# Kernel optimization log

Hardware: AMD Instinct MI355X
Metric: run time of the kernel (lower is better)

Reference implementation:

```python
import jax, jax.numpy as jnp
import numpy as np

N, IN_DIM, OUT_DIM, HEADS = 3072, 512, 64, 8
EDGE_PROB = 0.01
NEG_SLOPE = 0.2


def setup_inputs() -> dict:
    key = jax.random.key(0)
    k1, k2, k3, k4, k5 = jax.random.split(key, 5)
    x = jax.random.normal(k1, (N, IN_DIM), dtype=jnp.float32)
    # sparse-ish dense adjacency mask with self-loops
    adj = (jax.random.uniform(k2, (N, N)) < EDGE_PROB).astype(jnp.float32)
    adj = jnp.maximum(adj, jnp.eye(N, dtype=jnp.float32))
    W = jax.random.normal(k3, (HEADS, IN_DIM, OUT_DIM), dtype=jnp.float32) * 0.1
    a_src = jax.random.normal(k4, (HEADS, OUT_DIM), dtype=jnp.float32) * 0.1
    a_dst = jax.random.normal(k5, (HEADS, OUT_DIM), dtype=jnp.float32) * 0.1
    return {"x": x, "adj": adj, "W": W, "a_src": a_src, "a_dst": a_dst}


def reference(x, adj, W, a_src, a_dst):
    # per-head linear projection: [H, N, OUT]
    h = jnp.einsum("ni,hio->hno", x, W)
    # attention logits e_ij = LeakyReLU(a_src . h_i + a_dst . h_j)
    f_src = jnp.einsum("hno,ho->hn", h, a_src)  # [H, N]
    f_dst = jnp.einsum("hno,ho->hn", h, a_dst)  # [H, N]
    e = f_src[:, :, None] + f_dst[:, None, :]   # [H, N, N]
    e = jax.nn.leaky_relu(e, negative_slope=NEG_SLOPE)
    # mask non-edges, row-softmax over neighbors
    e = jnp.where(adj[None] > 0, e, jnp.float32(-1e9))
    att = jax.nn.softmax(e, axis=-1)             # [H, N, N]
    # aggregate neighbor features per head
    out = jnp.einsum("hij,hjo->hio", att, h)     # [H, N, OUT]
    # concat heads along feature dim -> [N, H*OUT]
    return out.transpose(1, 0, 2).reshape(N, HEADS * OUT_DIM)
```

## Files before the change

### kernel.cpp

```cpp
#include <hip/hip_runtime.h>

#define N_NODES 3072
#define IN_DIM 512
#define OUT_DIM 64
#define HEADS 8
#define NEG_SLOPE 0.2f
#define MAX_E 128

typedef __attribute__((ext_vector_type(8))) short bf16x8;
typedef __attribute__((ext_vector_type(4))) float f32x4;

#define XFRAG_TILES (N_NODES / 16)
#define KTILES (IN_DIM / 32)
#define XFRAG_THREADS (XFRAG_TILES * KTILES * 64)
#define WFRAG_THREADS (HEADS * KTILES * 4 * 64)

__device__ inline unsigned short f2bf(float f) {
    union { float f; unsigned u; } v; v.f = f;
    unsigned r = (v.u + 0x7FFF + ((v.u >> 16) & 1)) >> 16;
    return (unsigned short)r;
}

__global__ __launch_bounds__(256) void gat_prep(
    const float* __restrict__ x, const float* __restrict__ W,
    short* __restrict__ xfrag, short* __restrict__ wfrag) {
    int tid = blockIdx.x * 256 + threadIdx.x;
    if (tid < XFRAG_THREADS) {
        int lane = tid & 63;
        int kt = (tid >> 6) & (KTILES - 1);
        int rt = tid >> 10;
        int m = rt * 16 + (lane & 15);
        int k0 = kt * 32 + (lane >> 4) * 8;
        const float4* xp = (const float4*)(x + (size_t)m * IN_DIM + k0);
        float4 v0 = xp[0], v1 = xp[1];
        bf16x8 r;
        r[0] = (short)f2bf(v0.x); r[1] = (short)f2bf(v0.y);
        r[2] = (short)f2bf(v0.z); r[3] = (short)f2bf(v0.w);
        r[4] = (short)f2bf(v1.x); r[5] = (short)f2bf(v1.y);
        r[6] = (short)f2bf(v1.z); r[7] = (short)f2bf(v1.w);
        ((bf16x8*)xfrag)[tid] = r;
    } else {
        int t2 = tid - XFRAG_THREADS;
        if (t2 >= WFRAG_THREADS) return;
        int lane = t2 & 63;
        int c = (t2 >> 6) & 3;
        int kt = (t2 >> 8) & (KTILES - 1);
        int head = t2 >> 12;
        int n = c * 16 + (lane & 15);
        int k0 = kt * 32 + (lane >> 4) * 8;
        const float* wp = W + ((size_t)head * IN_DIM + k0) * OUT_DIM + n;
        bf16x8 r;
#pragma unroll
        for (int j = 0; j < 8; ++j) r[j] = (short)f2bf(wp[(size_t)j * OUT_DIM]);
        ((bf16x8*)wfrag)[t2] = r;
    }
}

__global__ __launch_bounds__(256) void gat_proj(
    const short* __restrict__ xfrag, const short* __restrict__ wfrag,
    const float* __restrict__ a_src, const float* __restrict__ a_dst,
    unsigned short* __restrict__ hb, float* __restrict__ fsrc, float* __restrict__ fdst) {
    __shared__ float hs[32][OUT_DIM + 1];

    const int t = threadIdx.x;
    const int lane = t & 63;
    const int w = t >> 6;
    const int head = blockIdx.y;
    const int m0 = blockIdx.x * 32;
    const int rt0 = blockIdx.x * 2;

    const bf16x8* xa = (const bf16x8*)xfrag + (size_t)rt0 * 16 * 64 + lane;
    const bf16x8* wb = (const bf16x8*)wfrag + ((size_t)head * KTILES * 4 + w) * 64 + lane;

    f32x4 acc0 = {0.f, 0.f, 0.f, 0.f};
    f32x4 acc1 = {0.f, 0.f, 0.f, 0.f};
#pragma unroll
    for (int kt = 0; kt < KTILES; ++kt) {
        bf16x8 a0 = xa[kt * 64];
        bf16x8 a1 = xa[(16 + kt) * 64];
        bf16x8 b  = wb[kt * 4 * 64];
        acc0 = __builtin_amdgcn_mfma_f32_16x16x32_bf16(a0, b, acc0, 0, 0, 0);
        acc1 = __builtin_amdgcn_mfma_f32_16x16x32_bf16(a1, b, acc1, 0, 0, 0);
    }

    const int col = w * 16 + (lane & 15);
    const int r0 = (lane >> 4) * 4;
    unsigned short* hp = hb + (size_t)m0 * (HEADS * OUT_DIM) + head * OUT_DIM + col;
#pragma unroll
    for (int i2 = 0; i2 < 4; ++i2) {
        hs[r0 + i2][col] = acc0[i2];
        hs[r0 + 16 + i2][col] = acc1[i2];
        hp[(size_t)(r0 + i2) * (HEADS * OUT_DIM)] = f2bf(acc0[i2]);
        hp[(size_t)(r0 + 16 + i2) * (HEADS * OUT_DIM)] = f2bf(acc1[i2]);
    }
    __syncthreads();

    {
        const float* av = (t < 128 ? a_src : a_dst) + head * OUT_DIM;
        const int tt = t & 127;
        const int row = tt >> 2, part = tt & 3;
        float s = 0.f;
#pragma unroll
        for (int n = 0; n < 16; ++n) s += hs[row][part * 16 + n] * av[part * 16 + n];
        s += __shfl_xor(s, 1, 64);
        s += __shfl_xor(s, 2, 64);
        if (part == 0) {
            float* dst = (t < 128 ? fsrc : fdst);
            dst[head * N_NODES + m0 + row] = s;
        }
    }
}

__global__ __launch_bounds__(256) void gat_agg(
    const float* __restrict__ adj, const unsigned short* __restrict__ hb,
    const float* __restrict__ fsrc, const float* __restrict__ fdst,
    float* __restrict__ out) {
    __shared__ int s_idx[MAX_E];
    __shared__ float s_p[HEADS][MAX_E];
    __shared__ int s_cnt;

    const int i = blockIdx.x;
    const int t = threadIdx.x;
    if (t == 0) s_cnt = 0;
    __syncthreads();

    const float4* arow4 = (const float4*)(adj + (size_t)i * N_NODES);
#pragma unroll
    for (int it = 0; it < 3; ++it) {
        const int jj = t + it * 256;
        float4 v = arow4[jj];
        const int j = jj * 4;
        if (v.x > 0.f) { int s = atomicAdd(&s_cnt, 1); if (s < MAX_E) s_idx[s] = j; }
        if (v.y > 0.f) { int s = atomicAdd(&s_cnt, 1); if (s < MAX_E) s_idx[s] = j + 1; }
        if (v.z > 0.f) { int s = atomicAdd(&s_cnt, 1); if (s < MAX_E) s_idx[s] = j + 2; }
        if (v.w > 0.f) { int s = atomicAdd(&s_cnt, 1); if (s < MAX_E) s_idx[s] = j + 3; }
    }
    __syncthreads();
    const int E = min(s_cnt, MAX_E);

    const int w = t >> 6;
    const int lane = t & 63;
    const int half = lane >> 5;
    const int sl = lane & 31;
    const int head = 2 * w + half;

    const float fi = fsrc[head * N_NODES + i];

    float m = -1e30f;
    for (int k = sl; k < E; k += 32) {
        float e = fi + fdst[head * N_NODES + s_idx[k]];
        e = e > 0.f ? e : NEG_SLOPE * e;
        s_p[head][k] = e;
        m = fmaxf(m, e);
    }
#pragma unroll
    for (int o = 16; o; o >>= 1) m = fmaxf(m, __shfl_xor(m, o, 64));

    float sum = 0.f;
    for (int k = sl; k < E; k += 32) {
        float p = __expf(s_p[head][k] - m);
        s_p[head][k] = p;
        sum += p;
    }
#pragma unroll
    for (int o = 16; o; o >>= 1) sum += __shfl_xor(sum, o, 64);
    const float inv = 1.f / sum;

    const unsigned short* hbase = hb + head * OUT_DIM + sl * 2;
    float a0 = 0.f, a1 = 0.f;
#pragma unroll 8
    for (int k = 0; k < E; ++k) {
        const int j = s_idx[k];
        const float p = s_p[head][k];
        const unsigned u = *(const unsigned*)(hbase + (size_t)j * (HEADS * OUT_DIM));
        a0 = fmaf(p, __uint_as_float(u << 16), a0);
        a1 = fmaf(p, __uint_as_float(u & 0xffff0000u), a1);
    }
    float2 r = {a0 * inv, a1 * inv};
    *(float2*)(out + (size_t)i * (HEADS * OUT_DIM) + head * OUT_DIM + sl * 2) = r;
}

extern "C" void kernel_launch(void* const* d_in, const int* in_sizes, int n_in,
                              void* d_out, int out_size, void* d_ws, size_t ws_size,
                              hipStream_t stream) {
    const float* x     = (const float*)d_in[0];
    const float* adj   = (const float*)d_in[1];
    const float* W     = (const float*)d_in[2];
    const float* a_src = (const float*)d_in[3];
    const float* a_dst = (const float*)d_in[4];
    float* out = (float*)d_out;

    float* fsrc = (float*)d_ws;
    float* fdst = fsrc + HEADS * N_NODES;
    unsigned short* hb = (unsigned short*)(fdst + HEADS * N_NODES);
    short* xfrag = (short*)(hb + (size_t)N_NODES * HEADS * OUT_DIM);
    short* wfrag = xfrag + (size_t)XFRAG_TILES * KTILES * 64 * 8;

    gat_prep<<<(XFRAG_THREADS + WFRAG_THREADS) / 256, 256, 0, stream>>>(
        x, W, xfrag, wfrag);
    gat_proj<<<dim3(N_NODES / 32, HEADS), 256, 0, stream>>>(
        xfrag, wfrag, a_src, a_dst, hb, fsrc, fdst);
    gat_agg<<<N_NODES, 256, 0, stream>>>(adj, hb, fsrc, fdst, out);
}
```

Baseline: 107.9 us.

## Split aggregation edges across wave halves with wider bf16 gathers and nontemporal adj loads

The neighbour-aggregation loop is remapped so each wave handles two heads with two edges in flight at once. Each lane now gathers four bf16 features per edge and walks half as many serial iterations, and the two halves are combined with a cross-lane shuffle. The softmax normalizer is passed through shared memory, and the adjacency row is read with nontemporal loads to avoid polluting the cache. The aim is to cut the latency of the dependent gather loop, at the cost of an extra shuffle reduction and predicated loads for odd edge counts.

```diff
diff --git a/kernel.cpp b/kernel.cpp
--- a/kernel.cpp
+++ b/kernel.cpp
@@ -9,6 +9,7 @@
 
 typedef __attribute__((ext_vector_type(8))) short bf16x8;
 typedef __attribute__((ext_vector_type(4))) float f32x4;
+typedef __attribute__((ext_vector_type(4))) float nfloat4;
 
 #define XFRAG_TILES (N_NODES / 16)
 #define KTILES (IN_DIM / 32)
@@ -20,6 +21,8 @@
     unsigned r = (v.u + 0x7FFF + ((v.u >> 16) & 1)) >> 16;
     return (unsigned short)r;
 }
+__device__ inline float bf_lo(unsigned u) { return __uint_as_float(u << 16); }
+__device__ inline float bf_hi(unsigned u) { return __uint_as_float(u & 0xffff0000u); }
 
 __global__ __launch_bounds__(256) void gat_prep(
     const float* __restrict__ x, const float* __restrict__ W,
@@ -117,6 +120,7 @@
     float* __restrict__ out) {
     __shared__ int s_idx[MAX_E];
     __shared__ float s_p[HEADS][MAX_E];
+    __shared__ float s_inv[HEADS];
     __shared__ int s_cnt;
 
     const int i = blockIdx.x;
@@ -124,11 +128,11 @@
     if (t == 0) s_cnt = 0;
     __syncthreads();
 
-    const float4* arow4 = (const float4*)(adj + (size_t)i * N_NODES);
+    const nfloat4* arow4 = (const nfloat4*)(adj + (size_t)i * N_NODES);
 #pragma unroll
     for (int it = 0; it < 3; ++it) {
         const int jj = t + it * 256;
-        float4 v = arow4[jj];
+        nfloat4 v = __builtin_nontemporal_load(arow4 + jj);
         const int j = jj * 4;
         if (v.x > 0.f) { int s = atomicAdd(&s_cnt, 1); if (s < MAX_E) s_idx[s] = j; }
         if (v.y > 0.f) { int s = atomicAdd(&s_cnt, 1); if (s < MAX_E) s_idx[s] = j + 1; }
@@ -140,44 +144,63 @@
 
     const int w = t >> 6;
     const int lane = t & 63;
-    const int half = lane >> 5;
-    const int sl = lane & 31;
-    const int head = 2 * w + half;
-
-    const float fi = fsrc[head * N_NODES + i];
-
-    float m = -1e30f;
-    for (int k = sl; k < E; k += 32) {
-        float e = fi + fdst[head * N_NODES + s_idx[k]];
-        e = e > 0.f ? e : NEG_SLOPE * e;
-        s_p[head][k] = e;
-        m = fmaxf(m, e);
-    }
-#pragma unroll
-    for (int o = 16; o; o >>= 1) m = fmaxf(m, __shfl_xor(m, o, 64));
-
-    float sum = 0.f;
-    for (int k = sl; k < E; k += 32) {
-        float p = __expf(s_p[head][k] - m);
-        s_p[head][k] = p;
-        sum += p;
-    }
-#pragma unroll
-    for (int o = 16; o; o >>= 1) sum += __shfl_xor(sum, o, 64);
-    const float inv = 1.f / sum;
-
-    const unsigned short* hbase = hb + head * OUT_DIM + sl * 2;
-    float a0 = 0.f, a1 = 0.f;
+
+    {
+        const int half = lane >> 5;
+        const int sl = lane & 31;
+        const int head = 2 * w + half;
+        const float fi = fsrc[head * N_NODES + i];
+
+        float m = -1e30f;
+        for (int k = sl; k < E; k += 32) {
+            float e = fi + fdst[head * N_NODES + s_idx[k]];
+            e = e > 0.f ? e : NEG_SLOPE * e;
+            s_p[head][k] = e;
+            m = fmaxf(m, e);
+        }
+#pragma unroll
+        for (int o = 16; o; o >>= 1) m = fmaxf(m, __shfl_xor(m, o, 64));
+
+        float sum = 0.f;
+        for (int k = sl; k < E; k += 32) {
+            float p = __expf(s_p[head][k] - m);
+            s_p[head][k] = p;
+            sum += p;
+        }
+#pragma unroll
+        for (int o = 16; o; o >>= 1) sum += __shfl_xor(sum, o, 64);
+        if (sl == 0) s_inv[head] = 1.f / sum;
+    }
+
+    const int e2 = lane >> 5;
+    const int hh = (lane >> 4) & 1;
+    const int d4 = lane & 15;
+    const int gh = 2 * w + hh;
+    const unsigned short* hbase = hb + gh * OUT_DIM + d4 * 4;
+
+    float a0 = 0.f, a1 = 0.f, a2 = 0.f, a3 = 0.f;
 #pragma unroll 8
-    for (int k = 0; k < E; ++k) {
-        const int j = s_idx[k];
-        const float p = s_p[head][k];
-        const unsigned u = *(const unsigned*)(hbase + (size_t)j * (HEADS * OUT_DIM));
-        a0 = fmaf(p, __uint_as_float(u << 16), a0);
-        a1 = fmaf(p, __uint_as_float(u & 0xffff0000u), a1);
-    }
-    float2 r = {a0 * inv, a1 * inv};
-    *(float2*)(out + (size_t)i * (HEADS * OUT_DIM) + head * OUT_DIM + sl * 2) = r;
+    for (int k = 0; k < E; k += 2) {
+        const int kk = k + e2;
+        const bool ok = kk < E;
+        const float p = ok ? s_p[gh][kk] : 0.f;
+        const int j = s_idx[ok ? kk : 0];
+        const uint2 u = *(const uint2*)(hbase + (size_t)j * (HEADS * OUT_DIM));
+        a0 = fmaf(p, bf_lo(u.x), a0);
+        a1 = fmaf(p, bf_hi(u.x), a1);
+        a2 = fmaf(p, bf_lo(u.y), a2);
+        a3 = fmaf(p, bf_hi(u.y), a3);
+    }
+    a0 += __shfl_xor(a0, 32, 64);
+    a1 += __shfl_xor(a1, 32, 64);
+    a2 += __shfl_xor(a2, 32, 64);
+    a3 += __shfl_xor(a3, 32, 64);
+
+    if (e2 == 0) {
+        const float inv = s_inv[gh];
+        float4 r = {a0 * inv, a1 * inv, a2 * inv, a3 * inv};
+        *(float4*)(out + (size_t)i * (HEADS * OUT_DIM) + gh * OUT_DIM + d4 * 4) = r;
+    }
 }
 
 extern "C" void kernel_launch(void* const* d_in, const int* in_sizes, int n_in,
```

Measured after the change: 113.3 us. 1.05x slower.
